# Optimization experiments

Hardware: AMD Instinct MI355X
Metric: run time of the kernel (lower is better)

Reference implementation:

```python
import jax, jax.numpy as jnp
import numpy as np

N_NODES = 50000


def gcn_conv(x, W, b, src, dst, n_nodes):
    """PyG-style GCNConv: add self-loops, symmetric deg^-1/2 norm, linear, aggregate."""
    # add self-loops
    loop = jnp.arange(n_nodes, dtype=src.dtype)
    s = jnp.concatenate([src, loop])  # source (j)
    d = jnp.concatenate([dst, loop])  # target (i)
    # degree computed on target index (PyG: deg = scatter ones over col)
    deg = jax.ops.segment_sum(jnp.ones_like(d, dtype=x.dtype), d, num_segments=n_nodes)
    dinv = jnp.where(deg > 0, jax.lax.rsqrt(deg), 0.0)
    norm = dinv[s] * dinv[d]  # [E+N]
    h = x @ W  # [N, out]
    msg = h[s] * norm[:, None]  # gather + scale, [E+N, out]
    out = jax.ops.segment_sum(msg, d, num_segments=n_nodes)  # scatter-add
    return out + b


def setup_inputs() -> dict:
    key = jax.random.key(0)
    k1, k2, k3, k4 = jax.random.split(key, 4)
    hidden = 128
    in_dim = hidden + 2
    E = 800000
    x = jax.random.normal(k1, (N_NODES, in_dim), dtype=jnp.float32)
    edge_index = jax.random.randint(k2, (2, E), 0, N_NODES, dtype=jnp.int64)
    # Glorot-ish init for weights
    W1 = jax.random.normal(k3, (in_dim, hidden), dtype=jnp.float32) / np.sqrt(in_dim)
    W2 = jax.random.normal(k4, (hidden, hidden), dtype=jnp.float32) / np.sqrt(hidden)
    b1 = jnp.zeros((hidden,), dtype=jnp.float32)
    b2 = jnp.zeros((hidden,), dtype=jnp.float32)
    return {"x": x, "edge_index": edge_index, "W1": W1, "b1": b1, "W2": W2, "b2": b2}


def reference(x, edge_index, W1, b1, W2, b2):
    src, dst = edge_index[0], edge_index[1]
    h = gcn_conv(x, W1, b1, src, dst, N_NODES)
    h = jax.nn.relu(h)
    h = gcn_conv(h, W2, b2, src, dst, N_NODES)
    h = jax.nn.relu(h)
    return h
```

## Files before the change

### kernel.cpp

```cpp
#include <hip/hip_runtime.h>
#include <hip/hip_fp16.h>


#define NNODES 50000


__global__ void count_kernel(const int* __restrict__ dst, int* __restrict__ cnt, int E) {
    int e = blockIdx.x * blockDim.x + threadIdx.x;
    if (e < E) atomicAdd(&cnt[dst[e]], 1);
}

__global__ __launch_bounds__(256) void scan_blocksum(const int* __restrict__ cnt,
                                                     int* __restrict__ bsum, int N) {
    __shared__ int ws[4];
    int i = blockIdx.x * 256 + threadIdx.x;
    int v = (i < N) ? cnt[i] : 0;
#pragma unroll
    for (int off = 1; off < 64; off <<= 1) v += __shfl_xor(v, off);
    int lane = threadIdx.x & 63, w = threadIdx.x >> 6;
    if (lane == 0) ws[w] = v;
    __syncthreads();
    if (threadIdx.x == 0) bsum[blockIdx.x] = ws[0] + ws[1] + ws[2] + ws[3];
}

__global__ __launch_bounds__(256) void scan_partials(const int* __restrict__ bsum,
                                                     int* __restrict__ boff,
                                                     int* __restrict__ row_start,
                                                     int NB, int N) {
    __shared__ int ws[4];
    int t = threadIdx.x;
    int v = (t < NB) ? bsum[t] : 0;
    int lane = t & 63, w = t >> 6;
    int inc = v;
#pragma unroll
    for (int off = 1; off < 64; off <<= 1) {
        int n = __shfl_up(inc, off);
        if (lane >= off) inc += n;
    }
    if (lane == 63) ws[w] = inc;
    __syncthreads();
    int woff = 0;
    for (int k = 0; k < w; ++k) woff += ws[k];
    int excl = woff + inc - v;
    if (t < NB) boff[t] = excl;
    if (t == NB - 1) row_start[N] = excl + v;
}

__global__ __launch_bounds__(256) void scan_final(const int* __restrict__ cnt,
                                                  const int* __restrict__ boff,
                                                  int* __restrict__ row_start,
                                                  float* __restrict__ dinv, int N) {
    __shared__ int ws[4];
    int i = blockIdx.x * 256 + threadIdx.x;
    int v = (i < N) ? cnt[i] : 0;
    int lane = threadIdx.x & 63, w = threadIdx.x >> 6;
    int inc = v;
#pragma unroll
    for (int off = 1; off < 64; off <<= 1) {
        int n = __shfl_up(inc, off);
        if (lane >= off) inc += n;
    }
    if (lane == 63) ws[w] = inc;
    __syncthreads();
    int woff = 0;
    for (int k = 0; k < w; ++k) woff += ws[k];
    if (i < N) {
        row_start[i] = boff[blockIdx.x] + woff + inc - v;
        dinv[i] = rsqrtf((float)(v + 1));
    }
}

__global__ __launch_bounds__(256) void scatter_kernel(const int* __restrict__ src,
                                                      const int* __restrict__ dst,
                                                      const int* __restrict__ row_start,
                                                      int* __restrict__ cursor,
                                                      int* __restrict__ esrc,
                                                      int E, int npo) {
    int owner = blockIdx.x & 7;
    int nblk  = gridDim.x >> 3;
    int bo    = blockIdx.x >> 3;
    int lo = owner * npo;
    int hi = lo + npo;
    for (int e = bo * 256 + threadIdx.x; e < E; e += nblk * 256) {
        int d = dst[e];
        if (d >= lo && d < hi) {
            int p = row_start[d] + atomicAdd(&cursor[d], 1);
            esrc[p] = src[e];
        }
    }
}


__global__ __launch_bounds__(256) void gemm_kernel(const float* __restrict__ A,
                                                   const float* __restrict__ W,
                                                   const float* __restrict__ dinv,
                                                   __half* __restrict__ Hs,
                                                   int M, int K) {
    constexpr int BM = 64, BN = 128, BK = 32, LDT = BM + 4;
    __shared__ float sAT[BK * LDT];
    __shared__ float sW[BK][BN];
    int t = threadIdx.x;
    int row0 = blockIdx.x * BM;
    int tx = t & 15;
    int ty = t >> 4;
    float acc[4][8] = {};

    float2 ra[4];
    float4 rw[4];
    int nk = (K + BK - 1) / BK;

#pragma unroll
    for (int j = 0; j < 4; ++j) {
        int s = t + 256 * j; int r = s >> 4; int c2 = s & 15;
        int gr = row0 + r, gk = c2 * 2;
        float2 v = make_float2(0.f, 0.f);
        if (gr < M) {
            if (gk + 1 < K)  v = *reinterpret_cast<const float2*>(&A[(size_t)gr * K + gk]);
            else if (gk < K) v.x = A[(size_t)gr * K + gk];
        }
        ra[j] = v;
    }
#pragma unroll
    for (int j = 0; j < 4; ++j) {
        int s = t + 256 * j; int r = s >> 5; int c4 = s & 31;
        float4 v = make_float4(0.f, 0.f, 0.f, 0.f);
        if (r < K) v = *reinterpret_cast<const float4*>(&W[(size_t)r * BN + c4 * 4]);
        rw[j] = v;
    }

    for (int kt = 0; kt < nk; ++kt) {
        __syncthreads();
#pragma unroll
        for (int j = 0; j < 4; ++j) {
            int s = t + 256 * j; int r = s >> 4; int c2 = s & 15;
            sAT[(2 * c2) * LDT + r]     = ra[j].x;
            sAT[(2 * c2 + 1) * LDT + r] = ra[j].y;
        }
#pragma unroll
        for (int j = 0; j < 4; ++j) {
            int s = t + 256 * j; int r = s >> 5; int c4 = s & 31;
            *reinterpret_cast<float4*>(&sW[r][c4 * 4]) = rw[j];
        }
        if (kt + 1 < nk) {
            int k0 = (kt + 1) * BK;
#pragma unroll
            for (int j = 0; j < 4; ++j) {
                int s = t + 256 * j; int r = s >> 4; int c2 = s & 15;
                int gr = row0 + r, gk = k0 + c2 * 2;
                float2 v = make_float2(0.f, 0.f);
                if (gr < M) {
                    if (gk + 1 < K)  v = *reinterpret_cast<const float2*>(&A[(size_t)gr * K + gk]);
                    else if (gk < K) v.x = A[(size_t)gr * K + gk];
                }
                ra[j] = v;
            }
#pragma unroll
            for (int j = 0; j < 4; ++j) {
                int s = t + 256 * j; int r = s >> 5; int c4 = s & 31;
                int gk = k0 + r;
                float4 v = make_float4(0.f, 0.f, 0.f, 0.f);
                if (gk < K) v = *reinterpret_cast<const float4*>(&W[(size_t)gk * BN + c4 * 4]);
                rw[j] = v;
            }
        }
        __syncthreads();
#pragma unroll 4
        for (int kk = 0; kk < BK; ++kk) {
            float4 av = *reinterpret_cast<const float4*>(&sAT[kk * LDT + ty * 4]);
            float4 b0 = *reinterpret_cast<const float4*>(&sW[kk][tx * 4]);
            float4 b1 = *reinterpret_cast<const float4*>(&sW[kk][64 + tx * 4]);
            float a[4] = {av.x, av.y, av.z, av.w};
#pragma unroll
            for (int i = 0; i < 4; ++i) {
                acc[i][0] = fmaf(a[i], b0.x, acc[i][0]);
                acc[i][1] = fmaf(a[i], b0.y, acc[i][1]);
                acc[i][2] = fmaf(a[i], b0.z, acc[i][2]);
                acc[i][3] = fmaf(a[i], b0.w, acc[i][3]);
                acc[i][4] = fmaf(a[i], b1.x, acc[i][4]);
                acc[i][5] = fmaf(a[i], b1.y, acc[i][5]);
                acc[i][6] = fmaf(a[i], b1.z, acc[i][6]);
                acc[i][7] = fmaf(a[i], b1.w, acc[i][7]);
            }
        }
    }
#pragma unroll
    for (int i = 0; i < 4; ++i) {
        int gr = row0 + ty * 4 + i;
        if (gr < M) {
            float di = dinv[gr];
            __half2 p0 = __floats2half2_rn(di * acc[i][0], di * acc[i][1]);
            __half2 p1 = __floats2half2_rn(di * acc[i][2], di * acc[i][3]);
            __half2 p2 = __floats2half2_rn(di * acc[i][4], di * acc[i][5]);
            __half2 p3 = __floats2half2_rn(di * acc[i][6], di * acc[i][7]);
            uint2 pk0, pk1;
            pk0.x = *reinterpret_cast<unsigned int*>(&p0);
            pk0.y = *reinterpret_cast<unsigned int*>(&p1);
            pk1.x = *reinterpret_cast<unsigned int*>(&p2);
            pk1.y = *reinterpret_cast<unsigned int*>(&p3);
            *reinterpret_cast<uint2*>(&Hs[(size_t)gr * BN + tx * 4])      = pk0;
            *reinterpret_cast<uint2*>(&Hs[(size_t)gr * BN + 64 + tx * 4]) = pk1;
        }
    }
}


__global__ __launch_bounds__(256) void agg_kernel(const __half* __restrict__ Hs,
                                                  const int* __restrict__ row_start,
                                                  const int* __restrict__ esrc,
                                                  const float* __restrict__ dinv,
                                                  const float* __restrict__ bias,
                                                  float* __restrict__ out, int N) {
    constexpr int F = 128;
    int node = blockIdx.x * 4 + (threadIdx.x >> 6);
    if (node >= N) return;
    int lane = threadIdx.x & 63;
    int c = lane & 31;
    int h = lane >> 5;
    int beg = row_start[node];
    int deg = row_start[node + 1] - beg;

    int spre = (lane < deg) ? esrc[beg + lane] : 0;

    float a0 = 0.f, a1 = 0.f, a2 = 0.f, a3 = 0.f;
    for (int j0 = 0; j0 < deg; j0 += 16) {
        int  sv[8];
        bool ok[8];
#pragma unroll
        for (int u = 0; u < 8; ++u) {
            int jj = j0 + 2 * u + h;
            ok[u] = (jj < deg);
            if (jj < 64) sv[u] = __shfl(spre, jj);
            else         sv[u] = ok[u] ? esrc[beg + jj] : 0;
        }
        uint2 v[8];
#pragma unroll
        for (int u = 0; u < 8; ++u) {
            v[u] = make_uint2(0u, 0u);
            if (ok[u])
                v[u] = *reinterpret_cast<const uint2*>(&Hs[(size_t)sv[u] * F + c * 4]);
        }
#pragma unroll
        for (int u = 0; u < 8; ++u) {
            __half2 h0 = *reinterpret_cast<__half2*>(&v[u].x);
            __half2 h1 = *reinterpret_cast<__half2*>(&v[u].y);
            float2 f0 = __half22float2(h0);
            float2 f1 = __half22float2(h1);
            a0 += f0.x; a1 += f0.y; a2 += f1.x; a3 += f1.y;
        }
    }
    a0 += __shfl_xor(a0, 32);
    a1 += __shfl_xor(a1, 32);
    a2 += __shfl_xor(a2, 32);
    a3 += __shfl_xor(a3, 32);

    if (h == 0) {
        uint2 sv2 = *reinterpret_cast<const uint2*>(&Hs[(size_t)node * F + c * 4]);
        __half2 s0 = *reinterpret_cast<__half2*>(&sv2.x);
        __half2 s1 = *reinterpret_cast<__half2*>(&sv2.y);
        float2 g0 = __half22float2(s0);
        float2 g1 = __half22float2(s1);
        float4 b = *reinterpret_cast<const float4*>(&bias[c * 4]);
        float di = dinv[node];
        float4 r;
        r.x = fmaxf(fmaf(di, a0 + g0.x, b.x), 0.f);
        r.y = fmaxf(fmaf(di, a1 + g0.y, b.y), 0.f);
        r.z = fmaxf(fmaf(di, a2 + g1.x, b.z), 0.f);
        r.w = fmaxf(fmaf(di, a3 + g1.y, b.w), 0.f);
        *reinterpret_cast<float4*>(&out[(size_t)node * F + c * 4]) = r;
    }
}


extern "C" void kernel_launch(void* const* d_in, const int* in_sizes, int n_in,
                              void* d_out, int out_size, void* d_ws, size_t ws_size,
                              hipStream_t stream) {
    const float* x  = (const float*)d_in[0];
    const int*   ei = (const int*)d_in[1];
    const float* W1 = (const float*)d_in[2];
    const float* b1 = (const float*)d_in[3];
    const float* W2 = (const float*)d_in[4];
    const float* b2 = (const float*)d_in[5];

    const int N   = NNODES;
    const int E   = in_sizes[1] / 2;
    const int K1  = in_sizes[0] / N;
    const int HID = in_sizes[3];
    const int NB  = (N + 255) / 256;
    const int NPO = (N + 7) / 8;

    const int* src = ei;
    const int* dst = ei + E;

    int*    cnt       = (int*)d_ws;
    int*    cursor    = cnt + N;
    int*    row_start = cursor + N;
    float*  dinv      = (float*)(row_start + N + 4);
    int*    bsum      = (int*)(dinv + N);
    int*    boff      = bsum + 256;
    int*    esrc      = boff + 256;
    __half* Hs        = (__half*)(esrc + E);
    float*  outf      = (float*)d_out;

    hipMemsetAsync(cnt, 0, sizeof(int) * 2 * (size_t)N, stream);

    count_kernel<<<(E + 255) / 256, 256, 0, stream>>>(dst, cnt, E);
    scan_blocksum<<<NB, 256, 0, stream>>>(cnt, bsum, N);
    scan_partials<<<1, 256, 0, stream>>>(bsum, boff, row_start, NB, N);
    scan_final<<<NB, 256, 0, stream>>>(cnt, boff, row_start, dinv, N);
    scatter_kernel<<<2048, 256, 0, stream>>>(src, dst, row_start, cursor, esrc, E, NPO);

    gemm_kernel<<<(N + 63) / 64, 256, 0, stream>>>(x, W1, dinv, Hs, N, K1);
    agg_kernel<<<(N + 3) / 4, 256, 0, stream>>>(Hs, row_start, esrc, dinv, b1, outf, N);
    gemm_kernel<<<(N + 63) / 64, 256, 0, stream>>>(outf, W2, dinv, Hs, N, HID);
    agg_kernel<<<(N + 3) / 4, 256, 0, stream>>>(Hs, row_start, esrc, dinv, b2, outf, N);
}
```

Baseline: 307.9 us.

## Switch GEMM to fp16 MFMA 16x16x32 with full W staged in shared memory

Replaces the fp32 FMA register-tiled GEMM with MFMA f32_16x16x32_f16 instructions. The whole W matrix is converted to fp16 and stored transposed in shared memory once per block, and A tiles are converted to fp16 on load. The aim is to cut the compute cost of the dense transform. In exchange, inputs lose precision to fp16, the register prefetch of the next tile is dropped, and the epilogue now writes scalar half values instead of vector stores.

```diff
diff --git a/kernel.cpp b/kernel.cpp
--- a/kernel.cpp
+++ b/kernel.cpp
@@ -3,6 +3,9 @@
 
 
 #define NNODES 50000
+
+typedef _Float16 f16x8 __attribute__((ext_vector_type(8)));
+typedef float    f32x4 __attribute__((ext_vector_type(4)));
 
 
 __global__ void count_kernel(const int* __restrict__ dst, int* __restrict__ cnt, int E) {
@@ -96,109 +99,69 @@
                                                    const float* __restrict__ dinv,
                                                    __half* __restrict__ Hs,
                                                    int M, int K) {
-    constexpr int BM = 64, BN = 128, BK = 32, LDT = BM + 4;
-    __shared__ float sAT[BK * LDT];
-    __shared__ float sW[BK][BN];
+    constexpr int BM = 64, BN = 128, BK = 32;
+    constexpr int LDA = 40;
+    constexpr int LDK = 168;
+    __shared__ _Float16 sA[BM * LDA];
+    __shared__ _Float16 sB[BN * LDK];
     int t = threadIdx.x;
+    int lane = t & 63;
+    int wv   = t >> 6;
     int row0 = blockIdx.x * BM;
-    int tx = t & 15;
-    int ty = t >> 4;
-    float acc[4][8] = {};
-
-    float2 ra[4];
-    float4 rw[4];
     int nk = (K + BK - 1) / BK;
 
-#pragma unroll
-    for (int j = 0; j < 4; ++j) {
-        int s = t + 256 * j; int r = s >> 4; int c2 = s & 15;
-        int gr = row0 + r, gk = c2 * 2;
-        float2 v = make_float2(0.f, 0.f);
-        if (gr < M) {
-            if (gk + 1 < K)  v = *reinterpret_cast<const float2*>(&A[(size_t)gr * K + gk]);
-            else if (gk < K) v.x = A[(size_t)gr * K + gk];
-        }
-        ra[j] = v;
-    }
-#pragma unroll
-    for (int j = 0; j < 4; ++j) {
-        int s = t + 256 * j; int r = s >> 5; int c4 = s & 31;
-        float4 v = make_float4(0.f, 0.f, 0.f, 0.f);
-        if (r < K) v = *reinterpret_cast<const float4*>(&W[(size_t)r * BN + c4 * 4]);
-        rw[j] = v;
-    }
+    {
+        int n = t & 127;
+        for (int kb = (t >> 7); kb < K; kb += 2)
+            sB[n * LDK + kb] = (_Float16)W[(size_t)kb * BN + n];
+        for (int kb = K + (t >> 7); kb < nk * BK; kb += 2)
+            sB[n * LDK + kb] = (_Float16)0.f;
+    }
+
+    f32x4 acc[8] = {};
+    int ar = t >> 2;
+    int ac = (t & 3) * 8;
 
     for (int kt = 0; kt < nk; ++kt) {
+        int k0 = kt * BK;
         __syncthreads();
-#pragma unroll
-        for (int j = 0; j < 4; ++j) {
-            int s = t + 256 * j; int r = s >> 4; int c2 = s & 15;
-            sAT[(2 * c2) * LDT + r]     = ra[j].x;
-            sAT[(2 * c2 + 1) * LDT + r] = ra[j].y;
-        }
-#pragma unroll
-        for (int j = 0; j < 4; ++j) {
-            int s = t + 256 * j; int r = s >> 5; int c4 = s & 31;
-            *reinterpret_cast<float4*>(&sW[r][c4 * 4]) = rw[j];
-        }
-        if (kt + 1 < nk) {
-            int k0 = (kt + 1) * BK;
+        {
+            int gr = row0 + ar;
+            f16x8 hv;
 #pragma unroll
             for (int j = 0; j < 4; ++j) {
-                int s = t + 256 * j; int r = s >> 4; int c2 = s & 15;
-                int gr = row0 + r, gk = k0 + c2 * 2;
+                int gk = k0 + ac + 2 * j;
                 float2 v = make_float2(0.f, 0.f);
                 if (gr < M) {
                     if (gk + 1 < K)  v = *reinterpret_cast<const float2*>(&A[(size_t)gr * K + gk]);
                     else if (gk < K) v.x = A[(size_t)gr * K + gk];
                 }
-                ra[j] = v;
+                hv[2 * j]     = (_Float16)v.x;
+                hv[2 * j + 1] = (_Float16)v.y;
             }
-#pragma unroll
-            for (int j = 0; j < 4; ++j) {
-                int s = t + 256 * j; int r = s >> 5; int c4 = s & 31;
-                int gk = k0 + r;
-                float4 v = make_float4(0.f, 0.f, 0.f, 0.f);
-                if (gk < K) v = *reinterpret_cast<const float4*>(&W[(size_t)gk * BN + c4 * 4]);
-                rw[j] = v;
-            }
+            *reinterpret_cast<f16x8*>(&sA[ar * LDA + ac]) = hv;
         }
         __syncthreads();
-#pragma unroll 4
-        for (int kk = 0; kk < BK; ++kk) {
-            float4 av = *reinterpret_cast<const float4*>(&sAT[kk * LDT + ty * 4]);
-            float4 b0 = *reinterpret_cast<const float4*>(&sW[kk][tx * 4]);
-            float4 b1 = *reinterpret_cast<const float4*>(&sW[kk][64 + tx * 4]);
-            float a[4] = {av.x, av.y, av.z, av.w};
-#pragma unroll
-            for (int i = 0; i < 4; ++i) {
-                acc[i][0] = fmaf(a[i], b0.x, acc[i][0]);
-                acc[i][1] = fmaf(a[i], b0.y, acc[i][1]);
-                acc[i][2] = fmaf(a[i], b0.z, acc[i][2]);
-                acc[i][3] = fmaf(a[i], b0.w, acc[i][3]);
-                acc[i][4] = fmaf(a[i], b1.x, acc[i][4]);
-                acc[i][5] = fmaf(a[i], b1.y, acc[i][5]);
-                acc[i][6] = fmaf(a[i], b1.z, acc[i][6]);
-                acc[i][7] = fmaf(a[i], b1.w, acc[i][7]);
-            }
-        }
-    }
-#pragma unroll
-    for (int i = 0; i < 4; ++i) {
-        int gr = row0 + ty * 4 + i;
+        f16x8 af = *reinterpret_cast<const f16x8*>(
+            &sA[(wv * 16 + (lane & 15)) * LDA + (lane >> 4) * 8]);
+#pragma unroll
+        for (int nf = 0; nf < 8; ++nf) {
+            f16x8 bf = *reinterpret_cast<const f16x8*>(
+                &sB[(nf * 16 + (lane & 15)) * LDK + k0 + (lane >> 4) * 8]);
+            acc[nf] = __builtin_amdgcn_mfma_f32_16x16x32_f16(af, bf, acc[nf], 0, 0, 0);
+        }
+    }
+
+    int ccol  = lane & 15;
+    int rbase = row0 + wv * 16 + (lane >> 4) * 4;
+#pragma unroll
+    for (int r = 0; r < 4; ++r) {
+        int gr = rbase + r;
         if (gr < M) {
             float di = dinv[gr];
-            __half2 p0 = __floats2half2_rn(di * acc[i][0], di * acc[i][1]);
-            __half2 p1 = __floats2half2_rn(di * acc[i][2], di * acc[i][3]);
-            __half2 p2 = __floats2half2_rn(di * acc[i][4], di * acc[i][5]);
-            __half2 p3 = __floats2half2_rn(di * acc[i][6], di * acc[i][7]);
-            uint2 pk0, pk1;
-            pk0.x = *reinterpret_cast<unsigned int*>(&p0);
-            pk0.y = *reinterpret_cast<unsigned int*>(&p1);
-            pk1.x = *reinterpret_cast<unsigned int*>(&p2);
-            pk1.y = *reinterpret_cast<unsigned int*>(&p3);
-            *reinterpret_cast<uint2*>(&Hs[(size_t)gr * BN + tx * 4])      = pk0;
-            *reinterpret_cast<uint2*>(&Hs[(size_t)gr * BN + 64 + tx * 4]) = pk1;
+#pragma unroll
+            for (int nf = 0; nf < 8; ++nf)
+                Hs[(size_t)gr * BN + nf * 16 + ccol] = __float2half(di * acc[nf][r]);
         }
     }
 }
```

Result: faster. 286.5 us (-7.0%).
